# Optimization experiments

Hardware: AMD Instinct MI355X
Metric: run time of the kernel (lower is better)

## Reference

```python
import jax, jax.numpy as jnp
import numpy as np

B, D, W = 8192, 64, 128  # batch, stack_depth, stack_width
HIDDEN = 128


def setup_inputs() -> dict:
    key = jax.random.key(0)
    ks = jax.random.split(key, 10)
    s = lambda n: 1.0 / np.sqrt(n)
    return {
        "stack": jax.random.normal(ks[0], (B, D, W), jnp.float32),
        "state_prev": jax.random.normal(ks[1], (B, 128), jnp.float32),
        "x_emb": jax.random.normal(ks[2], (B, HIDDEN), jnp.float32),
        "W_state": jax.random.normal(ks[3], (128, HIDDEN), jnp.float32) * s(128),
        "b_state": jnp.zeros((HIDDEN,), jnp.float32),
        "W_top": jax.random.normal(ks[4], (W, HIDDEN), jnp.float32) * s(W),
        "b_top": jnp.zeros((HIDDEN,), jnp.float32),
        "W_mem": jax.random.normal(ks[5], (3 * HIDDEN, 3), jnp.float32) * s(3 * HIDDEN),
        "b_mem": jnp.zeros((3,), jnp.float32),
        "W_buf": jax.random.normal(ks[6], (3 * HIDDEN, 128), jnp.float32) * s(3 * HIDDEN),
        "b_buf": jnp.zeros((128,), jnp.float32),
        "W_stateout": jax.random.normal(ks[7], (3 * HIDDEN, 128), jnp.float32) * s(3 * HIDDEN),
        "b_stateout": jnp.zeros((128,), jnp.float32),
    }


def reference(stack, state_prev, x_emb, W_state, b_state, W_top, b_top,
              W_mem, b_mem, W_buf, b_buf, W_stateout, b_stateout):
    stack_top = stack[:, 0]                                  # [B, W]
    state_emb = state_prev @ W_state + b_state               # [B, H]
    top_emb = stack_top @ W_top + b_top                      # [B, H]
    flat = jnp.concatenate([x_emb, state_emb, top_emb], -1)  # [B, 3H]
    logits_mem = flat @ W_mem + b_mem                        # [B, 3]
    logits_buf = flat @ W_buf + b_buf                        # [B, V]
    logits_state = flat @ W_stateout + b_stateout            # [B, S]
    action_probs = jax.nn.softmax(logits_mem, axis=-1)
    # differentiable stack update: push (shift down, duplicating top),
    # pop (shift up, zero-fill bottom), no-op; blended by action probs
    pushed = jnp.concatenate([stack[:, :1], stack[:, :-1]], axis=1)
    popped = jnp.concatenate([stack[:, 1:], jnp.zeros_like(stack[:, :1])], axis=1)
    p = action_probs[:, :, None, None]                       # [B, 3, 1, 1]
    stack_new = p[:, 0] * pushed + p[:, 1] * popped + p[:, 2] * stack
    next_state = jnp.tanh(logits_state)
    return stack_new, next_state, logits_buf, action_probs
```

## Files before the change

kernel.cpp:

```cpp
#include <hip/hip_runtime.h>
#include <math.h>

#define B_TOT 8192
#define D_ 64
#define W_ 128
#define H_ 128
#define NCOL 256

typedef float f32x4 __attribute__((ext_vector_type(4)));

#define WS_FWM     0
#define WS_FWMEM   98304
#define WS_BIASM   99456
#define WS_BIASMEM 99712

#define OUT_STACK 0
#define OUT_STATE 67108864UL
#define OUT_BUF   68157440UL
#define OUT_PROBS 69206016UL

#define NB_GEMM 512
#define NB_STEN 4096
#define BROWS 16
#define ACT_PAD 388

__global__ __launch_bounds__(256) void fold_kernel(
    const float* __restrict__ W_state, const float* __restrict__ b_state,
    const float* __restrict__ W_top,   const float* __restrict__ b_top,
    const float* __restrict__ W_mem,   const float* __restrict__ b_mem,
    const float* __restrict__ W_buf,   const float* __restrict__ b_buf,
    const float* __restrict__ W_stateout, const float* __restrict__ b_stateout,
    float* __restrict__ ws)
{
    int k = blockIdx.x;
    int j = threadIdx.x;
    int col = j & 127;
    const float* Whead = (j < 128) ? W_buf : W_stateout;
    const float* bhead = (j < 128) ? b_buf : b_stateout;
    float v;
    if (k < 128) {
        v = Whead[k*H_ + col];
    } else if (k < 256) {
        const float* a = W_state + (size_t)(k-128)*H_;
        float s = 0.f;
        for (int t = 0; t < 128; ++t) s += a[t] * Whead[(128+t)*H_ + col];
        v = s;
    } else {
        const float* a = W_top + (size_t)(k-256)*H_;
        float s = 0.f;
        for (int t = 0; t < 128; ++t) s += a[t] * Whead[(256+t)*H_ + col];
        v = s;
    }
    ws[WS_FWM + k*NCOL + j] = v;

    if (j < 3) {
        float v2;
        if (k < 128) v2 = W_mem[k*3 + j];
        else if (k < 256) {
            const float* a = W_state + (size_t)(k-128)*H_;
            float s = 0.f;
            for (int t = 0; t < 128; ++t) s += a[t] * W_mem[(128+t)*3 + j];
            v2 = s;
        } else {
            const float* a = W_top + (size_t)(k-256)*H_;
            float s = 0.f;
            for (int t = 0; t < 128; ++t) s += a[t] * W_mem[(256+t)*3 + j];
            v2 = s;
        }
        ws[WS_FWMEM + k*3 + j] = v2;
    }
    if (k == 0) {
        float s = bhead[col];
        for (int t = 0; t < 128; ++t)
            s += b_state[t]*Whead[(128+t)*H_ + col] + b_top[t]*Whead[(256+t)*H_ + col];
        ws[WS_BIASM + j] = s;
        if (j < 3) {
            float s2 = b_mem[j];
            for (int t = 0; t < 128; ++t)
                s2 += b_state[t]*W_mem[(128+t)*3 + j] + b_top[t]*W_mem[(256+t)*3 + j];
            ws[WS_BIASMEM + j] = s2;
        }
    }
}

__global__ __launch_bounds__(256) void main_kernel(
    const float* __restrict__ stack, const float* __restrict__ state_prev,
    const float* __restrict__ x_emb, const float* __restrict__ ws,
    float* __restrict__ out)
{
    int tid = threadIdx.x;
    __shared__ float act[BROWS * ACT_PAD];
    __shared__ float psh[2][3];

    if (blockIdx.x < NB_GEMM) {
        int b0 = blockIdx.x * BROWS;

        #pragma unroll
        for (int s = 0; s < 3; ++s) {
            #pragma unroll
            for (int it = 0; it < 2; ++it) {
                int idx = it*256 + tid;
                int r   = idx >> 5;
                int kk  = (idx & 31) << 2;
                const float* src;
                if (s == 0)      src = x_emb      + (size_t)(b0+r)*H_;
                else if (s == 1) src = state_prev + (size_t)(b0+r)*H_;
                else             src = stack      + (size_t)(b0+r)*(D_*W_);
                f32x4 v = *(const f32x4*)(src + kk);
                *(f32x4*)(act + r*ACT_PAD + s*128 + kk) = v;
            }
        }
        __syncthreads();

        int rg = tid & 3;
        int cg = tid >> 2;
        const float* __restrict__ FW = ws + WS_FWM;
        f32x4 bj = *(const f32x4*)(ws + WS_BIASM + 4*cg);
        float acc[4][4];
        #pragma unroll
        for (int r = 0; r < 4; ++r) {
            acc[r][0] = bj.x; acc[r][1] = bj.y; acc[r][2] = bj.z; acc[r][3] = bj.w;
        }
        const float* a0p = act + (4*rg+0)*ACT_PAD;
        const float* a1p = act + (4*rg+1)*ACT_PAD;
        const float* a2p = act + (4*rg+2)*ACT_PAD;
        const float* a3p = act + (4*rg+3)*ACT_PAD;

        #pragma unroll 4
        for (int k = 0; k < 384; ++k) {
            f32x4 w = *(const f32x4*)(FW + (size_t)k*NCOL + 4*cg);
            float a0 = a0p[k], a1 = a1p[k], a2 = a2p[k], a3 = a3p[k];
            acc[0][0] += a0*w.x; acc[0][1] += a0*w.y; acc[0][2] += a0*w.z; acc[0][3] += a0*w.w;
            acc[1][0] += a1*w.x; acc[1][1] += a1*w.y; acc[1][2] += a1*w.z; acc[1][3] += a1*w.w;
            acc[2][0] += a2*w.x; acc[2][1] += a2*w.y; acc[2][2] += a2*w.z; acc[2][3] += a2*w.w;
            acc[3][0] += a3*w.x; acc[3][1] += a3*w.y; acc[3][2] += a3*w.z; acc[3][3] += a3*w.w;
        }

        #pragma unroll
        for (int r = 0; r < 4; ++r) {
            size_t row = (size_t)(b0 + 4*rg + r);
            if (cg < 32) {
                f32x4 o = {acc[r][0], acc[r][1], acc[r][2], acc[r][3]};
                __builtin_nontemporal_store(o, (f32x4*)(out + OUT_BUF + row*H_ + 4*cg));
            } else {
                f32x4 o = {tanhf(acc[r][0]), tanhf(acc[r][1]),
                           tanhf(acc[r][2]), tanhf(acc[r][3])};
                __builtin_nontemporal_store(o, (f32x4*)(out + OUT_STATE + row*H_ + (4*cg - 128)));
            }
        }
    } else {
        int blk  = blockIdx.x - NB_GEMM;
        int wv   = tid >> 6;
        int lane = tid & 63;

        if ((wv & 1) == 0) {
            int bb = blk*2 + (wv >> 1);
            const float* __restrict__ FM = ws + WS_FWMEM;
            float a0 = 0.f, a1 = 0.f, a2 = 0.f;
            int kbase = lane * 6;
            #pragma unroll
            for (int jj = 0; jj < 6; ++jj) {
                int k = kbase + jj;
                float x;
                if (k < 128)      x = x_emb[(size_t)bb*H_ + k];
                else if (k < 256) x = state_prev[(size_t)bb*H_ + (k-128)];
                else              x = stack[(size_t)bb*(D_*W_) + (k-256)];
                a0 += x * FM[k*3+0];
                a1 += x * FM[k*3+1];
                a2 += x * FM[k*3+2];
            }
            #pragma unroll
            for (int m = 1; m < 64; m <<= 1) {
                a0 += __shfl_xor(a0, m);
                a1 += __shfl_xor(a1, m);
                a2 += __shfl_xor(a2, m);
            }
            if (lane == 0) {
                float l0 = a0 + ws[WS_BIASMEM+0];
                float l1 = a1 + ws[WS_BIASMEM+1];
                float l2 = a2 + ws[WS_BIASMEM+2];
                float mm = fmaxf(l0, fmaxf(l1, l2));
                float e0 = __expf(l0-mm), e1 = __expf(l1-mm), e2 = __expf(l2-mm);
                float inv = 1.f / (e0+e1+e2);
                int ro = wv >> 1;
                psh[ro][0] = e0*inv; psh[ro][1] = e1*inv; psh[ro][2] = e2*inv;
                __builtin_nontemporal_store(e0*inv, out + OUT_PROBS + (size_t)bb*3 + 0);
                __builtin_nontemporal_store(e1*inv, out + OUT_PROBS + (size_t)bb*3 + 1);
                __builtin_nontemporal_store(e2*inv, out + OUT_PROBS + (size_t)bb*3 + 2);
            }
        }
        __syncthreads();

        int w4  = tid & 31;
        int seg = (tid >> 5) & 3;
        int bo  = tid >> 7;
        size_t b = (size_t)blk * 2 + bo;
        float p0 = psh[bo][0], p1 = psh[bo][1], p2 = psh[bo][2];

        const f32x4* sp = (const f32x4*)(stack + b*(D_*W_)) + w4;
        f32x4*       op = (f32x4*)(out + OUT_STACK + b*(D_*W_)) + w4;

        int d0 = seg * 16;
        f32x4 cur  = sp[(size_t)d0*32];
        f32x4 prev = (d0 == 0) ? cur : sp[(size_t)(d0-1)*32];
        #pragma unroll
        for (int h = 0; h < 2; ++h) {
            int base = d0 + h*8;
            f32x4 nx[8];
            #pragma unroll
            for (int i = 0; i < 8; ++i) {
                int d = base + i + 1;
                if (d < 64) nx[i] = sp[(size_t)d*32];
                else        nx[i] = (f32x4){0.f, 0.f, 0.f, 0.f};
            }
            #pragma unroll
            for (int i = 0; i < 8; ++i) {
                int d = base + i;
                f32x4 o = p0*prev + p1*nx[i] + p2*cur;
                __builtin_nontemporal_store(o, op + (size_t)d*32);
                prev = cur; cur = nx[i];
            }
        }
    }
}

extern "C" void kernel_launch(void* const* d_in, const int* in_sizes, int n_in,
                              void* d_out, int out_size, void* d_ws, size_t ws_size,
                              hipStream_t stream) {
    const float* stack      = (const float*)d_in[0];
    const float* state_prev = (const float*)d_in[1];
    const float* x_emb      = (const float*)d_in[2];
    const float* W_state    = (const float*)d_in[3];
    const float* b_state    = (const float*)d_in[4];
    const float* W_top      = (const float*)d_in[5];
    const float* b_top      = (const float*)d_in[6];
    const float* W_mem      = (const float*)d_in[7];
    const float* b_mem      = (const float*)d_in[8];
    const float* W_buf      = (const float*)d_in[9];
    const float* b_buf      = (const float*)d_in[10];
    const float* W_stateout = (const float*)d_in[11];
    const float* b_stateout = (const float*)d_in[12];
    float* out = (float*)d_out;
    float* ws  = (float*)d_ws;

    hipLaunchKernelGGL(fold_kernel, dim3(384), dim3(256), 0, stream,
        W_state, b_state, W_top, b_top, W_mem, b_mem,
        W_buf, b_buf, W_stateout, b_stateout, ws);
    hipLaunchKernelGGL(main_kernel, dim3(NB_GEMM + NB_STEN), dim3(256), 0, stream,
        stack, state_prev, x_emb, ws, out);
}
```

Baseline: 120.7 us.

## Split GEMM and stencil into separate kernels, compute action probs in GEMM

Splits the fused kernel into a GEMM kernel and a stencil kernel. The GEMM kernel now also computes the 3-way softmax action probabilities from its shared-memory activations and writes them to the output. The stencil kernel reads those probabilities back from global memory instead of recomputing them per block. This removes the redundant per-block logits reduction and the block-wide sync from the stencil path, at the cost of an extra launch and serializing the GEMM before the stencil instead of overlapping them.

```diff
diff --git a/kernel.cpp b/kernel.cpp
--- a/kernel.cpp
+++ b/kernel.cpp
@@ -83,143 +83,143 @@
     }
 }
 
-__global__ __launch_bounds__(256) void main_kernel(
+__global__ __launch_bounds__(256) void gemm_kernel(
     const float* __restrict__ stack, const float* __restrict__ state_prev,
     const float* __restrict__ x_emb, const float* __restrict__ ws,
     float* __restrict__ out)
 {
     int tid = threadIdx.x;
     __shared__ float act[BROWS * ACT_PAD];
-    __shared__ float psh[2][3];
-
-    if (blockIdx.x < NB_GEMM) {
-        int b0 = blockIdx.x * BROWS;
-
-        #pragma unroll
-        for (int s = 0; s < 3; ++s) {
-            #pragma unroll
-            for (int it = 0; it < 2; ++it) {
-                int idx = it*256 + tid;
-                int r   = idx >> 5;
-                int kk  = (idx & 31) << 2;
-                const float* src;
-                if (s == 0)      src = x_emb      + (size_t)(b0+r)*H_;
-                else if (s == 1) src = state_prev + (size_t)(b0+r)*H_;
-                else             src = stack      + (size_t)(b0+r)*(D_*W_);
-                f32x4 v = *(const f32x4*)(src + kk);
-                *(f32x4*)(act + r*ACT_PAD + s*128 + kk) = v;
-            }
-        }
-        __syncthreads();
-
-        int rg = tid & 3;
-        int cg = tid >> 2;
-        const float* __restrict__ FW = ws + WS_FWM;
-        f32x4 bj = *(const f32x4*)(ws + WS_BIASM + 4*cg);
-        float acc[4][4];
-        #pragma unroll
-        for (int r = 0; r < 4; ++r) {
-            acc[r][0] = bj.x; acc[r][1] = bj.y; acc[r][2] = bj.z; acc[r][3] = bj.w;
-        }
-        const float* a0p = act + (4*rg+0)*ACT_PAD;
-        const float* a1p = act + (4*rg+1)*ACT_PAD;
-        const float* a2p = act + (4*rg+2)*ACT_PAD;
-        const float* a3p = act + (4*rg+3)*ACT_PAD;
-
-        #pragma unroll 4
-        for (int k = 0; k < 384; ++k) {
-            f32x4 w = *(const f32x4*)(FW + (size_t)k*NCOL + 4*cg);
-            float a0 = a0p[k], a1 = a1p[k], a2 = a2p[k], a3 = a3p[k];
-            acc[0][0] += a0*w.x; acc[0][1] += a0*w.y; acc[0][2] += a0*w.z; acc[0][3] += a0*w.w;
-            acc[1][0] += a1*w.x; acc[1][1] += a1*w.y; acc[1][2] += a1*w.z; acc[1][3] += a1*w.w;
-            acc[2][0] += a2*w.x; acc[2][1] += a2*w.y; acc[2][2] += a2*w.z; acc[2][3] += a2*w.w;
-            acc[3][0] += a3*w.x; acc[3][1] += a3*w.y; acc[3][2] += a3*w.z; acc[3][3] += a3*w.w;
-        }
-
-        #pragma unroll
-        for (int r = 0; r < 4; ++r) {
-            size_t row = (size_t)(b0 + 4*rg + r);
-            if (cg < 32) {
-                f32x4 o = {acc[r][0], acc[r][1], acc[r][2], acc[r][3]};
-                __builtin_nontemporal_store(o, (f32x4*)(out + OUT_BUF + row*H_ + 4*cg));
-            } else {
-                f32x4 o = {tanhf(acc[r][0]), tanhf(acc[r][1]),
-                           tanhf(acc[r][2]), tanhf(acc[r][3])};
-                __builtin_nontemporal_store(o, (f32x4*)(out + OUT_STATE + row*H_ + (4*cg - 128)));
-            }
-        }
-    } else {
-        int blk  = blockIdx.x - NB_GEMM;
-        int wv   = tid >> 6;
-        int lane = tid & 63;
-
-        if ((wv & 1) == 0) {
-            int bb = blk*2 + (wv >> 1);
-            const float* __restrict__ FM = ws + WS_FWMEM;
-            float a0 = 0.f, a1 = 0.f, a2 = 0.f;
-            int kbase = lane * 6;
-            #pragma unroll
-            for (int jj = 0; jj < 6; ++jj) {
-                int k = kbase + jj;
-                float x;
-                if (k < 128)      x = x_emb[(size_t)bb*H_ + k];
-                else if (k < 256) x = state_prev[(size_t)bb*H_ + (k-128)];
-                else              x = stack[(size_t)bb*(D_*W_) + (k-256)];
-                a0 += x * FM[k*3+0];
-                a1 += x * FM[k*3+1];
-                a2 += x * FM[k*3+2];
-            }
-            #pragma unroll
-            for (int m = 1; m < 64; m <<= 1) {
-                a0 += __shfl_xor(a0, m);
-                a1 += __shfl_xor(a1, m);
-                a2 += __shfl_xor(a2, m);
-            }
-            if (lane == 0) {
-                float l0 = a0 + ws[WS_BIASMEM+0];
-                float l1 = a1 + ws[WS_BIASMEM+1];
-                float l2 = a2 + ws[WS_BIASMEM+2];
-                float mm = fmaxf(l0, fmaxf(l1, l2));
-                float e0 = __expf(l0-mm), e1 = __expf(l1-mm), e2 = __expf(l2-mm);
-                float inv = 1.f / (e0+e1+e2);
-                int ro = wv >> 1;
-                psh[ro][0] = e0*inv; psh[ro][1] = e1*inv; psh[ro][2] = e2*inv;
-                __builtin_nontemporal_store(e0*inv, out + OUT_PROBS + (size_t)bb*3 + 0);
-                __builtin_nontemporal_store(e1*inv, out + OUT_PROBS + (size_t)bb*3 + 1);
-                __builtin_nontemporal_store(e2*inv, out + OUT_PROBS + (size_t)bb*3 + 2);
-            }
-        }
-        __syncthreads();
-
-        int w4  = tid & 31;
-        int seg = (tid >> 5) & 3;
-        int bo  = tid >> 7;
-        size_t b = (size_t)blk * 2 + bo;
-        float p0 = psh[bo][0], p1 = psh[bo][1], p2 = psh[bo][2];
-
-        const f32x4* sp = (const f32x4*)(stack + b*(D_*W_)) + w4;
-        f32x4*       op = (f32x4*)(out + OUT_STACK + b*(D_*W_)) + w4;
-
-        int d0 = seg * 16;
-        f32x4 cur  = sp[(size_t)d0*32];
-        f32x4 prev = (d0 == 0) ? cur : sp[(size_t)(d0-1)*32];
-        #pragma unroll
-        for (int h = 0; h < 2; ++h) {
-            int base = d0 + h*8;
-            f32x4 nx[8];
-            #pragma unroll
-            for (int i = 0; i < 8; ++i) {
-                int d = base + i + 1;
-                if (d < 64) nx[i] = sp[(size_t)d*32];
-                else        nx[i] = (f32x4){0.f, 0.f, 0.f, 0.f};
-            }
-            #pragma unroll
-            for (int i = 0; i < 8; ++i) {
-                int d = base + i;
-                f32x4 o = p0*prev + p1*nx[i] + p2*cur;
-                __builtin_nontemporal_store(o, op + (size_t)d*32);
-                prev = cur; cur = nx[i];
-            }
+    int b0 = blockIdx.x * BROWS;
+
+    #pragma unroll
+    for (int s = 0; s < 3; ++s) {
+        #pragma unroll
+        for (int it = 0; it < 2; ++it) {
+            int idx = it*256 + tid;
+            int r   = idx >> 5;
+            int kk  = (idx & 31) << 2;
+            const float* src;
+            if (s == 0)      src = x_emb      + (size_t)(b0+r)*H_;
+            else if (s == 1) src = state_prev + (size_t)(b0+r)*H_;
+            else             src = stack      + (size_t)(b0+r)*(D_*W_);
+            f32x4 v = *(const f32x4*)(src + kk);
+            *(f32x4*)(act + r*ACT_PAD + s*128 + kk) = v;
+        }
+    }
+    __syncthreads();
+
+    int rg = tid & 3;
+    int cg = tid >> 2;
+    const float* __restrict__ FW = ws + WS_FWM;
+    f32x4 bj = *(const f32x4*)(ws + WS_BIASM + 4*cg);
+    float acc[4][4];
+    #pragma unroll
+    for (int r = 0; r < 4; ++r) {
+        acc[r][0] = bj.x; acc[r][1] = bj.y; acc[r][2] = bj.z; acc[r][3] = bj.w;
+    }
+    const float* a0p = act + (4*rg+0)*ACT_PAD;
+    const float* a1p = act + (4*rg+1)*ACT_PAD;
+    const float* a2p = act + (4*rg+2)*ACT_PAD;
+    const float* a3p = act + (4*rg+3)*ACT_PAD;
+
+    #pragma unroll 4
+    for (int k = 0; k < 384; ++k) {
+        f32x4 w = *(const f32x4*)(FW + (size_t)k*NCOL + 4*cg);
+        float a0 = a0p[k], a1 = a1p[k], a2 = a2p[k], a3 = a3p[k];
+        acc[0][0] += a0*w.x; acc[0][1] += a0*w.y; acc[0][2] += a0*w.z; acc[0][3] += a0*w.w;
+        acc[1][0] += a1*w.x; acc[1][1] += a1*w.y; acc[1][2] += a1*w.z; acc[1][3] += a1*w.w;
+        acc[2][0] += a2*w.x; acc[2][1] += a2*w.y; acc[2][2] += a2*w.z; acc[2][3] += a2*w.w;
+        acc[3][0] += a3*w.x; acc[3][1] += a3*w.y; acc[3][2] += a3*w.z; acc[3][3] += a3*w.w;
+    }
+
+    #pragma unroll
+    for (int r = 0; r < 4; ++r) {
+        size_t row = (size_t)(b0 + 4*rg + r);
+        if (cg < 32) {
+            f32x4 o = {acc[r][0], acc[r][1], acc[r][2], acc[r][3]};
+            __builtin_nontemporal_store(o, (f32x4*)(out + OUT_BUF + row*H_ + 4*cg));
+        } else {
+            f32x4 o = {tanhf(acc[r][0]), tanhf(acc[r][1]),
+                       tanhf(acc[r][2]), tanhf(acc[r][3])};
+            __builtin_nontemporal_store(o, (f32x4*)(out + OUT_STATE + row*H_ + (4*cg - 128)));
+        }
+    }
+
+    int wv = tid >> 6, lane = tid & 63;
+    const float* __restrict__ FM = ws + WS_FWMEM;
+    float fm[6][3];
+    #pragma unroll
+    for (int jj = 0; jj < 6; ++jj) {
+        int k = lane*6 + jj;
+        fm[jj][0] = FM[k*3+0]; fm[jj][1] = FM[k*3+1]; fm[jj][2] = FM[k*3+2];
+    }
+    for (int r = wv; r < BROWS; r += 4) {
+        const float* ap = act + r*ACT_PAD + lane*6;
+        float a0 = 0.f, a1 = 0.f, a2 = 0.f;
+        #pragma unroll
+        for (int jj = 0; jj < 6; ++jj) {
+            float x = ap[jj];
+            a0 += x * fm[jj][0];
+            a1 += x * fm[jj][1];
+            a2 += x * fm[jj][2];
+        }
+        #pragma unroll
+        for (int m = 1; m < 64; m <<= 1) {
+            a0 += __shfl_xor(a0, m);
+            a1 += __shfl_xor(a1, m);
+            a2 += __shfl_xor(a2, m);
+        }
+        if (lane == 0) {
+            float l0 = a0 + ws[WS_BIASMEM+0];
+            float l1 = a1 + ws[WS_BIASMEM+1];
+            float l2 = a2 + ws[WS_BIASMEM+2];
+            float mm = fmaxf(l0, fmaxf(l1, l2));
+            float e0 = __expf(l0-mm), e1 = __expf(l1-mm), e2 = __expf(l2-mm);
+            float inv = 1.f / (e0+e1+e2);
+            size_t bb = (size_t)(b0 + r);
+            out[OUT_PROBS + bb*3 + 0] = e0*inv;
+            out[OUT_PROBS + bb*3 + 1] = e1*inv;
+            out[OUT_PROBS + bb*3 + 2] = e2*inv;
+        }
+    }
+}
+
+__global__ __launch_bounds__(256) void stencil_kernel(
+    const float* __restrict__ stack, float* __restrict__ out)
+{
+    int tid = threadIdx.x;
+    int w4  = tid & 31;
+    int seg = (tid >> 5) & 3;
+    int bo  = tid >> 7;
+    size_t b = (size_t)blockIdx.x * 2 + bo;
+
+    float p0 = out[OUT_PROBS + b*3 + 0];
+    float p1 = out[OUT_PROBS + b*3 + 1];
+    float p2 = out[OUT_PROBS + b*3 + 2];
+
+    const f32x4* sp = (const f32x4*)(stack + b*(D_*W_)) + w4;
+    f32x4*       op = (f32x4*)(out + OUT_STACK + b*(D_*W_)) + w4;
+
+    int d0 = seg * 16;
+    f32x4 cur  = sp[(size_t)d0*32];
+    f32x4 prev = (d0 == 0) ? cur : sp[(size_t)(d0-1)*32];
+    #pragma unroll
+    for (int h = 0; h < 2; ++h) {
+        int base = d0 + h*8;
+        f32x4 nx[8];
+        #pragma unroll
+        for (int i = 0; i < 8; ++i) {
+            int d = base + i + 1;
+            if (d < 64) nx[i] = sp[(size_t)d*32];
+            else        nx[i] = (f32x4){0.f, 0.f, 0.f, 0.f};
+        }
+        #pragma unroll
+        for (int i = 0; i < 8; ++i) {
+            int d = base + i;
+            f32x4 o = p0*prev + p1*nx[i] + p2*cur;
+            __builtin_nontemporal_store(o, op + (size_t)d*32);
+            prev = cur; cur = nx[i];
         }
     }
 }
@@ -246,6 +246,8 @@
     hipLaunchKernelGGL(fold_kernel, dim3(384), dim3(256), 0, stream,
         W_state, b_state, W_top, b_top, W_mem, b_mem,
         W_buf, b_buf, W_stateout, b_stateout, ws);
-    hipLaunchKernelGGL(main_kernel, dim3(NB_GEMM + NB_STEN), dim3(256), 0, stream,
+    hipLaunchKernelGGL(gemm_kernel, dim3(NB_GEMM), dim3(256), 0, stream,
         stack, state_prev, x_emb, ws, out);
-}
+    hipLaunchKernelGGL(stencil_kernel, dim3(NB_STEN), dim3(256), 0, stream,
+        stack, out);
+}
```

After: 141.7 us. 1.17x slower.
